# Kernel tuning notes

Measured on AMD Instinct MI355X. Metric: run time of the kernel, lower is better.

## Reference

```python
import jax, jax.numpy as jnp
import numpy as np
from jax import lax


def _conv(x, w, b):
    # 3x3 conv, stride 1, padding 1 == SAME; NCHW / OIHW layout like torch
    y = lax.conv_general_dilated(x, w, window_strides=(1, 1), padding='SAME',
                                 dimension_numbers=('NCHW', 'OIHW', 'NCHW'))
    return y + b[None, :, None, None]


def _maxpool2(x):
    return lax.reduce_window(x, -jnp.inf, lax.max, (1, 1, 2, 2), (1, 1, 2, 2), 'VALID')


def _upsample2(x):
    # nearest-neighbor upsample, scale factor 2
    return jnp.repeat(jnp.repeat(x, 2, axis=2), 2, axis=3)


def setup_inputs() -> dict:
    key = jax.random.key(0)
    ks = jax.random.split(key, 10)
    B, H, W = 128, 128, 128
    n_codes, d = 512, 32
    s = 0.1
    return {
        'x': jax.random.normal(ks[0], (B, 1, H, W), jnp.float32),
        'w1': jax.random.normal(ks[1], (16, 1, 3, 3), jnp.float32) * s,
        'b1': jnp.zeros((16,), jnp.float32),
        'w2': jax.random.normal(ks[2], (32, 16, 3, 3), jnp.float32) * s,
        'b2': jnp.zeros((32,), jnp.float32),
        'codebook': jax.random.normal(ks[3], (n_codes, d), jnp.float32),
        'w3': jax.random.normal(ks[4], (16, 32, 3, 3), jnp.float32) * s,
        'b3': jnp.zeros((16,), jnp.float32),
        'w4': jax.random.normal(ks[5], (1, 16, 3, 3), jnp.float32) * s,
        'b4': jnp.zeros((1,), jnp.float32),
    }


def reference(x, w1, b1, w2, b2, codebook, w3, b3, w4, b4):
    # encoder
    h = jax.nn.gelu(_maxpool2(_conv(x, w1, b1)), approximate=False)
    h = _maxpool2(_conv(h, w2, b2))  # [B, 32, H/4, W/4]
    B, C, Hq, Wq = h.shape

    # VectorQuantize: euclidean nearest-code lookup on flattened fmap
    z = h.transpose(0, 2, 3, 1).reshape(B, Hq * Wq, C)  # [B, N, d]
    d2 = ((z * z).sum(-1, keepdims=True)
          - 2.0 * jnp.einsum('bnc,kc->bnk', z, codebook)
          + (codebook * codebook).sum(-1))  # [B, N, K]
    idx = jnp.argmin(d2, axis=-1)  # [B, N]
    quant = codebook[idx]  # [B, N, d]
    commit_loss = jnp.mean((lax.stop_gradient(quant) - z) ** 2)
    indices = idx.reshape(B, Hq, Wq)

    # decoder: NOTE the source discards the quantized output (x_flat) and
    # keeps feeding the pre-quantization fmap h forward; we match that.
    g = jax.nn.gelu(_conv(_upsample2(h), w3, b3), approximate=False)
    out = jnp.clip(_conv(_upsample2(g), w4, b4), -1.0, 1.0)
    return out, indices, commit_loss
```

## Files before the change

### kernel.cpp

```cpp
#include <hip/hip_runtime.h>
#include <math.h>

__device__ __forceinline__ float gelu_f(float x) {
    return 0.5f * x * (1.0f + erff(x * 0.7071067811865476f));
}

__global__ __launch_bounds__(256) void k_prep(const float* __restrict__ cb,
                                              float* __restrict__ ccp) {
    const int k = blockIdx.x * 256 + threadIdx.x;
    if (k < 512) {
        const float* row = cb + k * 32;
        float s = 0.f;
#pragma unroll
        for (int c = 0; c < 32; ++c) s += row[c] * row[c];
        ccp[k] = s;
    }
}

__global__ __launch_bounds__(256) void k_conv1(const float* __restrict__ x,
                                               const float* __restrict__ w1,
                                               const float* __restrict__ b1,
                                               float* __restrict__ h1) {
    __shared__ float xs[34 * 38];
    const int blk = blockIdx.x;
    const int b = blk >> 4;
    const int tile = blk & 15;
    const int ti = (tile >> 2) << 4, tj = (tile & 3) << 4;
    const int t = threadIdx.x;
    const float* xb = x + b * 16384;
    for (int i = t; i < 34 * 34; i += 256) {
        const int r = i / 34, c = i % 34;
        const int gr = 2 * ti - 1 + r, gc = 2 * tj - 1 + c;
        const float v = ((unsigned)gr < 128u && (unsigned)gc < 128u) ? xb[gr * 128 + gc] : 0.f;
        xs[r * 38 + (c & 1) * 19 + (c >> 1)] = v;
    }
    __syncthreads();
    const int jj = t & 15, ii = t >> 4;
    float pat[4][4];
#pragma unroll
    for (int r = 0; r < 4; r++) {
        const int row = (2 * ii + r) * 38;
        pat[r][0] = xs[row + jj];
        pat[r][1] = xs[row + 19 + jj];
        pat[r][2] = xs[row + jj + 1];
        pat[r][3] = xs[row + 20 + jj];
    }
    const int obase = b * 65536 + (ti + ii) * 64 + (tj + jj);
#pragma unroll 2
    for (int co = 0; co < 16; co++) {
        const float* wr = w1 + co * 9;
        float w[9];
#pragma unroll
        for (int k = 0; k < 9; k++) w[k] = wr[k];
        float s00 = 0.f, s01 = 0.f, s10 = 0.f, s11 = 0.f;
#pragma unroll
        for (int ty = 0; ty < 3; ty++)
#pragma unroll
            for (int tx = 0; tx < 3; tx++) {
                const float wv = w[ty * 3 + tx];
                s00 += wv * pat[ty][tx];
                s01 += wv * pat[ty][tx + 1];
                s10 += wv * pat[ty + 1][tx];
                s11 += wv * pat[ty + 1][tx + 1];
            }
        const float m = fmaxf(fmaxf(s00, s01), fmaxf(s10, s11)) + b1[co];
        h1[obase + co * 4096] = gelu_f(m);
    }
}

__global__ __launch_bounds__(256) void k_conv2(const float* __restrict__ h1,
                                               const float* __restrict__ w2,
                                               const float* __restrict__ b2,
                                               float* __restrict__ h) {
    __shared__ float hs[16 * 360];
    const int blk = blockIdx.x;
    const int b = blk >> 4;
    const int tile = blk & 15;
    const int ti = (tile >> 2) << 3, tj = (tile & 3) << 3;
    const int t = threadIdx.x;
    const float* h1b = h1 + b * 65536;
    for (int i = t; i < 16 * 324; i += 256) {
        const int ci = i / 324, rc = i % 324, r = rc / 18, c = rc % 18;
        const int gr = 2 * ti - 1 + r, gc = 2 * tj - 1 + c;
        const float v = ((unsigned)gr < 64u && (unsigned)gc < 64u) ? h1b[ci * 4096 + gr * 64 + gc] : 0.f;
        hs[ci * 360 + r * 20 + (c & 1) * 10 + (c >> 1)] = v;
    }
    __syncthreads();
    const int co0 = __builtin_amdgcn_readfirstlane((t >> 6) << 3);
    const int lane = t & 63;
    const int irow = lane >> 3, j = lane & 7;
    float acc[8][4];
#pragma unroll
    for (int q = 0; q < 8; q++) { acc[q][0] = 0.f; acc[q][1] = 0.f; acc[q][2] = 0.f; acc[q][3] = 0.f; }
    const float* wbase = w2 + co0 * 144;
#pragma unroll 4
    for (int ci = 0; ci < 16; ci++) {
        float pat[4][4];
#pragma unroll
        for (int r = 0; r < 4; r++) {
            const int row = ci * 360 + (2 * irow + r) * 20;
            pat[r][0] = hs[row + j];
            pat[r][1] = hs[row + 10 + j];
            pat[r][2] = hs[row + j + 1];
            pat[r][3] = hs[row + 11 + j];
        }
#pragma unroll
        for (int q = 0; q < 8; q++) {
            const float* wr = wbase + q * 144 + ci * 9;
            float w[9];
#pragma unroll
            for (int k = 0; k < 9; k++) w[k] = wr[k];
#pragma unroll
            for (int ty = 0; ty < 3; ty++)
#pragma unroll
                for (int tx = 0; tx < 3; tx++) {
                    const float wv = w[ty * 3 + tx];
                    acc[q][0] += wv * pat[ty][tx];
                    acc[q][1] += wv * pat[ty][tx + 1];
                    acc[q][2] += wv * pat[ty + 1][tx];
                    acc[q][3] += wv * pat[ty + 1][tx + 1];
                }
        }
    }
    float* hb = h + (b * 32 + co0) * 1024 + (ti + irow) * 32 + tj + j;
#pragma unroll
    for (int q = 0; q < 8; q++) {
        hb[q * 1024] = fmaxf(fmaxf(acc[q][0], acc[q][1]), fmaxf(acc[q][2], acc[q][3])) + b2[co0 + q];
    }
}

__global__ __launch_bounds__(256) void k_vq_part(const float* __restrict__ h,
                                                 const float* __restrict__ cb,
                                                 const float* __restrict__ ccp,
                                                 float2* __restrict__ part) {
    const int blk = blockIdx.x;
    const int nchunk = blk >> 2, ks = blk & 3;
    const int t = threadIdx.x;
    const int n = nchunk * 256 + t;
    const int b = n >> 10, pos = n & 1023;
    const float* hb = h + b * 32768 + pos;
    float z[32];
    float zz = 0.f;
#pragma unroll
    for (int c = 0; c < 32; ++c) {
        z[c] = hb[c * 1024];
        zz += z[c] * z[c];
    }
    const int kbase = ks << 7;
    const float* cbb = cb + (kbase << 5);
    const float* ccb = ccp + kbase;
    float bd = 3.4e38f;
    int bk = 0;
#pragma unroll 1
    for (int kk = 0; kk < 128; kk += 2) {
        const float* r0 = cbb + (kk << 5);
        const float* r1 = r0 + 32;
        float d0a = 0.f, d0b = 0.f, d1a = 0.f, d1b = 0.f;
#pragma unroll
        for (int c = 0; c < 32; c += 2) {
            d0a += z[c] * r0[c];
            d0b += z[c + 1] * r0[c + 1];
            d1a += z[c] * r1[c];
            d1b += z[c + 1] * r1[c + 1];
        }
        const float dot0 = d0a + d0b;
        const float dot1 = d1a + d1b;
        const float e0 = (zz - 2.f * dot0) + ccb[kk];
        const float e1 = (zz - 2.f * dot1) + ccb[kk + 1];
        if (e0 < bd) { bd = e0; bk = kbase + kk; }
        if (e1 < bd) { bd = e1; bk = kbase + kk + 1; }
    }
    part[ks * 131072 + n] = make_float2(bd, (float)bk);
}

__global__ __launch_bounds__(256) void k_vq_comb(const float2* __restrict__ part,
                                                 float* __restrict__ idx_out,
                                                 float* __restrict__ partials) {
    const int t = threadIdx.x;
    const int n = blockIdx.x * 256 + t;
    float2 p0 = part[n];
    float2 p1 = part[131072 + n];
    float2 p2 = part[262144 + n];
    float2 p3 = part[393216 + n];
    float bd = p0.x;
    float bk = p0.y;
    if (p1.x < bd) { bd = p1.x; bk = p1.y; }
    if (p2.x < bd) { bd = p2.x; bk = p2.y; }
    if (p3.x < bd) { bd = p3.x; bk = p3.y; }
    idx_out[n] = bk;
    __shared__ float red[256];
    red[t] = bd;
    __syncthreads();
    for (int off = 128; off > 0; off >>= 1) {
        if (t < off) red[t] += red[t + off];
        __syncthreads();
    }
    if (t == 0) partials[blockIdx.x] = red[0];
}

__global__ __launch_bounds__(256) void k_conv3(const float* __restrict__ h,
                                               const float* __restrict__ w3,
                                               const float* __restrict__ b3,
                                               float* __restrict__ g) {
    __shared__ float hS[16 * 350];
    const int blk = blockIdx.x;
    const int b = blk >> 2, strip = blk & 3;
    const int i0 = strip * 8;
    const int t = threadIdx.x;
    const int co0 = __builtin_amdgcn_readfirstlane((t >> 6) << 2);
    const int lane = t & 63;
    const int rp = lane >> 3, cg = lane & 7;
    float acc[4][2][8];
#pragma unroll
    for (int cq = 0; cq < 4; cq++)
#pragma unroll
        for (int rr = 0; rr < 2; rr++)
#pragma unroll
            for (int u = 0; u < 8; u++) acc[cq][rr][u] = 0.f;
    const float* hb = h + b * 32768;
#pragma unroll 1
    for (int chunk = 0; chunk < 2; chunk++) {
        __syncthreads();
        for (int i = t; i < 16 * 340; i += 256) {
            const int cil = i / 340, rc = i % 340, r = rc / 34, c = rc % 34;
            const int gr = i0 - 1 + r, gc = c - 1;
            const float v = ((unsigned)gr < 32u && (unsigned)gc < 32u)
                ? hb[(chunk * 16 + cil) * 1024 + gr * 32 + gc] : 0.f;
            hS[cil * 350 + r * 35 + c] = v;
        }
        __syncthreads();
#pragma unroll 2
        for (int cil = 0; cil < 16; cil++) {
            const int ci = chunk * 16 + cil;
            float colr[3][6];
#pragma unroll
            for (int rr = 0; rr < 3; rr++) {
                const int rowb = cil * 350 + (rp + rr) * 35 + 4 * cg;
#pragma unroll
                for (int u = 0; u < 6; u++) colr[rr][u] = hS[rowb + u];
            }
#pragma unroll
            for (int cq = 0; cq < 4; cq++) {
                const float* wr = w3 + ((co0 + cq) * 32 + ci) * 9;
                float w[9];
#pragma unroll
                for (int k = 0; k < 9; k++) w[k] = wr[k];
                const float T00 = w[0], T01 = w[1], T02 = w[2];
                const float T10 = w[3] + w[6], T11 = w[4] + w[7], T12 = w[5] + w[8];
                const float T20 = w[0] + w[3], T21 = w[1] + w[4], T22 = w[2] + w[5];
                const float T30 = w[6], T31 = w[7], T32 = w[8];
                const float E01 = T01 + T02, O00 = T00 + T01;
                const float E11 = T11 + T12, O10 = T10 + T11;
                const float E21 = T21 + T22, O20 = T20 + T21;
                const float E31 = T31 + T32, O30 = T30 + T31;
#pragma unroll
                for (int mm = 0; mm < 4; mm++) {
                    acc[cq][0][2 * mm]     += T00 * colr[0][mm] + E01 * colr[0][mm + 1] + T10 * colr[1][mm] + E11 * colr[1][mm + 1];
                    acc[cq][0][2 * mm + 1] += O00 * colr[0][mm + 1] + T02 * colr[0][mm + 2] + O10 * colr[1][mm + 1] + T12 * colr[1][mm + 2];
                    acc[cq][1][2 * mm]     += T20 * colr[1][mm] + E21 * colr[1][mm + 1] + T30 * colr[2][mm] + E31 * colr[2][mm + 1];
                    acc[cq][1][2 * mm + 1] += O20 * colr[1][mm + 1] + T22 * colr[1][mm + 2] + O30 * colr[2][mm + 1] + T32 * colr[2][mm + 2];
                }
            }
        }
    }
    const int p_e = strip * 16 + 2 * rp;
#pragma unroll
    for (int cq = 0; cq < 4; cq++) {
        const float bias = b3[co0 + cq];
        float* gb = g + (b * 16 + co0 + cq) * 4096 + p_e * 64 + 8 * cg;
#pragma unroll
        for (int rr = 0; rr < 2; rr++) {
            float4 v0, v1;
            v0.x = gelu_f(acc[cq][rr][0] + bias);
            v0.y = gelu_f(acc[cq][rr][1] + bias);
            v0.z = gelu_f(acc[cq][rr][2] + bias);
            v0.w = gelu_f(acc[cq][rr][3] + bias);
            v1.x = gelu_f(acc[cq][rr][4] + bias);
            v1.y = gelu_f(acc[cq][rr][5] + bias);
            v1.z = gelu_f(acc[cq][rr][6] + bias);
            v1.w = gelu_f(acc[cq][rr][7] + bias);
            *(float4*)(gb + rr * 64) = v0;
            *(float4*)(gb + rr * 64 + 4) = v1;
        }
    }
}

__global__ __launch_bounds__(256) void k_conv4(const float* __restrict__ g,
                                               const float* __restrict__ w4,
                                               const float* __restrict__ b4,
                                               float* __restrict__ out) {
    __shared__ float gS[8 * 690];
    const int blk = blockIdx.x;
    const int b = blk >> 3, strip = blk & 7;
    const int i0 = strip * 8;
    const int t = threadIdx.x;
    const int rp = t >> 5, cg = t & 31;
    float acc[2][4];
#pragma unroll
    for (int rr = 0; rr < 2; rr++)
#pragma unroll
        for (int u = 0; u < 4; u++) acc[rr][u] = 0.f;
    const float* gbs = g + b * 65536;
#pragma unroll 1
    for (int chunk = 0; chunk < 2; chunk++) {
        __syncthreads();
        for (int i = t; i < 8 * 660; i += 256) {
            const int cil = i / 660, rc = i % 660, r = rc / 66, c = rc % 66;
            const int gr = i0 - 1 + r, gc = c - 1;
            const float v = ((unsigned)gr < 64u && (unsigned)gc < 64u)
                ? gbs[(chunk * 8 + cil) * 4096 + gr * 64 + gc] : 0.f;
            gS[cil * 690 + r * 69 + c] = v;
        }
        __syncthreads();
#pragma unroll 2
        for (int cil = 0; cil < 8; cil++) {
            const int ci = chunk * 8 + cil;
            float colv[3][4];
#pragma unroll
            for (int rr = 0; rr < 3; rr++) {
                const int rowb = cil * 690 + (rp + rr) * 69 + 2 * cg;
#pragma unroll
                for (int u = 0; u < 4; u++) colv[rr][u] = gS[rowb + u];
            }
            const float* wr = w4 + ci * 9;
            float w[9];
#pragma unroll
            for (int k = 0; k < 9; k++) w[k] = wr[k];
            const float T00 = w[0], T01 = w[1], T02 = w[2];
            const float T10 = w[3] + w[6], T11 = w[4] + w[7], T12 = w[5] + w[8];
            const float T20 = w[0] + w[3], T21 = w[1] + w[4], T22 = w[2] + w[5];
            const float T30 = w[6], T31 = w[7], T32 = w[8];
            const float E01 = T01 + T02, O00 = T00 + T01;
            const float E11 = T11 + T12, O10 = T10 + T11;
            const float E21 = T21 + T22, O20 = T20 + T21;
            const float E31 = T31 + T32, O30 = T30 + T31;
#pragma unroll
            for (int mm = 0; mm < 2; mm++) {
                acc[0][2 * mm]     += T00 * colv[0][mm] + E01 * colv[0][mm + 1] + T10 * colv[1][mm] + E11 * colv[1][mm + 1];
                acc[0][2 * mm + 1] += O00 * colv[0][mm + 1] + T02 * colv[0][mm + 2] + O10 * colv[1][mm + 1] + T12 * colv[1][mm + 2];
                acc[1][2 * mm]     += T20 * colv[1][mm] + E21 * colv[1][mm + 1] + T30 * colv[2][mm] + E31 * colv[2][mm + 1];
                acc[1][2 * mm + 1] += O20 * colv[1][mm + 1] + T22 * colv[1][mm + 2] + O30 * colv[2][mm + 1] + T32 * colv[2][mm + 2];
            }
        }
    }
    const float bias = b4[0];
    const int p_e = strip * 16 + 2 * rp;
    float* ob = out + b * 16384 + p_e * 128 + 4 * cg;
#pragma unroll
    for (int rr = 0; rr < 2; rr++) {
        float4 v;
        v.x = fminf(fmaxf(acc[rr][0] + bias, -1.f), 1.f);
        v.y = fminf(fmaxf(acc[rr][1] + bias, -1.f), 1.f);
        v.z = fminf(fmaxf(acc[rr][2] + bias, -1.f), 1.f);
        v.w = fminf(fmaxf(acc[rr][3] + bias, -1.f), 1.f);
        *(float4*)(ob + rr * 128) = v;
    }
}

__global__ __launch_bounds__(256) void k_reduce(const float* __restrict__ partials,
                                                float* __restrict__ loss) {
    __shared__ float red[256];
    const int t = threadIdx.x;
    float s = 0.f;
    for (int i = t; i < 512; i += 256) s += partials[i];
    red[t] = s;
    __syncthreads();
    for (int off = 128; off > 0; off >>= 1) {
        if (t < off) red[t] += red[t + off];
        __syncthreads();
    }
    if (t == 0) loss[0] = red[0] * (1.0f / 4194304.0f);
}

extern "C" void kernel_launch(void* const* d_in, const int* in_sizes, int n_in,
                              void* d_out, int out_size, void* d_ws, size_t ws_size,
                              hipStream_t stream) {
    const float* x  = (const float*)d_in[0];
    const float* w1 = (const float*)d_in[1];
    const float* b1 = (const float*)d_in[2];
    const float* w2 = (const float*)d_in[3];
    const float* b2 = (const float*)d_in[4];
    const float* cb = (const float*)d_in[5];
    const float* w3 = (const float*)d_in[6];
    const float* b3 = (const float*)d_in[7];
    const float* w4 = (const float*)d_in[8];
    const float* b4 = (const float*)d_in[9];

    float* ws = (float*)d_ws;
    float* h1 = ws;
    float* h  = ws + 8388608;
    float* g  = h1;
    float2* part = (float2*)ws;
    float* ccp = ws + 12582912;
    float* pa  = ws + 12583424;
    float* outp = (float*)d_out;

    k_prep<<<2, 256, 0, stream>>>(cb, ccp);
    k_conv1<<<2048, 256, 0, stream>>>(x, w1, b1, h1);
    k_conv2<<<2048, 256, 0, stream>>>(h1, w2, b2, h);
    k_vq_part<<<2048, 256, 0, stream>>>(h, cb, ccp, part);
    k_vq_comb<<<512, 256, 0, stream>>>(part, outp + 2097152, pa);
    k_conv3<<<512, 256, 0, stream>>>(h, w3, b3, g);
    k_conv4<<<1024, 256, 0, stream>>>(g, w4, b4, outp);
    k_reduce<<<1, 256, 0, stream>>>(pa, outp + 2228224);
}
```

Before: 243.0 us.

## Precompute folded upsample-conv weights and use packed float2 FMAs in conv2/VQ

Moves the folding of the 3x3 weights into upsample-aware 4x4 combinations for conv3 and conv4 out of the inner loops and into the prep kernel, which writes them to workspace. conv3 and conv4 then load 16 precomputed values per channel instead of 9 raw weights plus adds. conv2 and the VQ distance loop switch to 2-wide float vectors so the compiler can emit packed FP32 FMAs. This adds workspace traffic for the transformed weights and relies on the compiler actually emitting packed math.

Result: no change. 239.0 us (-1.7%).

```diff
diff --git a/kernel.cpp b/kernel.cpp
--- a/kernel.cpp
+++ b/kernel.cpp
@@ -1,19 +1,49 @@
 #include <hip/hip_runtime.h>
 #include <math.h>
 
+typedef float f32x2 __attribute__((ext_vector_type(2)));
+
 __device__ __forceinline__ float gelu_f(float x) {
     return 0.5f * x * (1.0f + erff(x * 0.7071067811865476f));
 }
 
 __global__ __launch_bounds__(256) void k_prep(const float* __restrict__ cb,
-                                              float* __restrict__ ccp) {
-    const int k = blockIdx.x * 256 + threadIdx.x;
-    if (k < 512) {
-        const float* row = cb + k * 32;
+                                              const float* __restrict__ w3,
+                                              const float* __restrict__ w4,
+                                              float* __restrict__ ccp,
+                                              float* __restrict__ w3t,
+                                              float* __restrict__ w4t) {
+    const int id = blockIdx.x * 256 + threadIdx.x;
+    {
+        const float* row = cb + id * 32;
         float s = 0.f;
 #pragma unroll
         for (int c = 0; c < 32; ++c) s += row[c] * row[c];
-        ccp[k] = s;
+        ccp[id] = s;
+    }
+    {
+        const float* w = w3 + id * 9;
+        const float T00 = w[0], T01 = w[1], T02 = w[2];
+        const float T10 = w[3] + w[6], T11 = w[4] + w[7], T12 = w[5] + w[8];
+        const float T20 = w[0] + w[3], T21 = w[1] + w[4], T22 = w[2] + w[5];
+        const float T30 = w[6], T31 = w[7], T32 = w[8];
+        float* o = w3t + id * 16;
+        o[0] = T00; o[1] = T00 + T01; o[2] = T01 + T02; o[3] = T02;
+        o[4] = T10; o[5] = T10 + T11; o[6] = T11 + T12; o[7] = T12;
+        o[8] = T20; o[9] = T20 + T21; o[10] = T21 + T22; o[11] = T22;
+        o[12] = T30; o[13] = T30 + T31; o[14] = T31 + T32; o[15] = T32;
+    }
+    if (id < 16) {
+        const float* w = w4 + id * 9;
+        const float T00 = w[0], T01 = w[1], T02 = w[2];
+        const float T10 = w[3] + w[6], T11 = w[4] + w[7], T12 = w[5] + w[8];
+        const float T20 = w[0] + w[3], T21 = w[1] + w[4], T22 = w[2] + w[5];
+        const float T30 = w[6], T31 = w[7], T32 = w[8];
+        float* o = w4t + id * 16;
+        o[0] = T00; o[1] = T00 + T01; o[2] = T01 + T02; o[3] = T02;
+        o[4] = T10; o[5] = T10 + T11; o[6] = T11 + T12; o[7] = T12;
+        o[8] = T20; o[9] = T20 + T21; o[10] = T21 + T22; o[11] = T22;
+        o[12] = T30; o[13] = T30 + T31; o[14] = T31 + T32; o[15] = T32;
     }
 }
 
@@ -89,20 +119,23 @@
     const int co0 = __builtin_amdgcn_readfirstlane((t >> 6) << 3);
     const int lane = t & 63;
     const int irow = lane >> 3, j = lane & 7;
-    float acc[8][4];
-#pragma unroll
-    for (int q = 0; q < 8; q++) { acc[q][0] = 0.f; acc[q][1] = 0.f; acc[q][2] = 0.f; acc[q][3] = 0.f; }
+    f32x2 A[8], B[8];
+#pragma unroll
+    for (int q = 0; q < 8; q++) { A[q] = (f32x2){0.f, 0.f}; B[q] = (f32x2){0.f, 0.f}; }
     const float* wbase = w2 + co0 * 144;
 #pragma unroll 4
     for (int ci = 0; ci < 16; ci++) {
-        float pat[4][4];
+        f32x2 P[4][3];
 #pragma unroll
         for (int r = 0; r < 4; r++) {
             const int row = ci * 360 + (2 * irow + r) * 20;
-            pat[r][0] = hs[row + j];
-            pat[r][1] = hs[row + 10 + j];
-            pat[r][2] = hs[row + j + 1];
-            pat[r][3] = hs[row + 11 + j];
+            const float e0 = hs[row + j];
+            const float o0 = hs[row + 10 + j];
+            const float e1 = hs[row + j + 1];
+            const float o1 = hs[row + 11 + j];
+            P[r][0] = (f32x2){e0, o0};
+            P[r][1] = (f32x2){o0, e1};
+            P[r][2] = (f32x2){e1, o1};
         }
 #pragma unroll
         for (int q = 0; q < 8; q++) {
@@ -115,17 +148,15 @@
 #pragma unroll
                 for (int tx = 0; tx < 3; tx++) {
                     const float wv = w[ty * 3 + tx];
-                    acc[q][0] += wv * pat[ty][tx];
-                    acc[q][1] += wv * pat[ty][tx + 1];
-                    acc[q][2] += wv * pat[ty + 1][tx];
-                    acc[q][3] += wv * pat[ty + 1][tx + 1];
+                    A[q] += P[ty][tx] * wv;
+                    B[q] += P[ty + 1][tx] * wv;
                 }
         }
     }
     float* hb = h + (b * 32 + co0) * 1024 + (ti + irow) * 32 + tj + j;
 #pragma unroll
     for (int q = 0; q < 8; q++) {
-        hb[q * 1024] = fmaxf(fmaxf(acc[q][0], acc[q][1]), fmaxf(acc[q][2], acc[q][3])) + b2[co0 + q];
+        hb[q * 1024] = fmaxf(fmaxf(A[q].x, A[q].y), fmaxf(B[q].x, B[q].y)) + b2[co0 + q];
     }
 }
 
@@ -146,6 +177,9 @@
         z[c] = hb[c * 1024];
         zz += z[c] * z[c];
     }
+    f32x2 z2[16];
+#pragma unroll
+    for (int i = 0; i < 16; ++i) z2[i] = (f32x2){z[2 * i], z[2 * i + 1]};
     const int kbase = ks << 7;
     const float* cbb = cb + (kbase << 5);
     const float* ccb = ccp + kbase;
@@ -153,18 +187,17 @@
     int bk = 0;
 #pragma unroll 1
     for (int kk = 0; kk < 128; kk += 2) {
-        const float* r0 = cbb + (kk << 5);
-        const float* r1 = r0 + 32;
-        float d0a = 0.f, d0b = 0.f, d1a = 0.f, d1b = 0.f;
-#pragma unroll
-        for (int c = 0; c < 32; c += 2) {
-            d0a += z[c] * r0[c];
-            d0b += z[c + 1] * r0[c + 1];
-            d1a += z[c] * r1[c];
-            d1b += z[c + 1] * r1[c + 1];
-        }
-        const float dot0 = d0a + d0b;
-        const float dot1 = d1a + d1b;
+        const f32x2* r0 = (const f32x2*)(cbb + (kk << 5));
+        const f32x2* r1 = (const f32x2*)(cbb + (kk << 5) + 32);
+        f32x2 D0 = (f32x2){0.f, 0.f};
+        f32x2 D1 = (f32x2){0.f, 0.f};
+#pragma unroll
+        for (int i = 0; i < 16; ++i) {
+            D0 += z2[i] * r0[i];
+            D1 += z2[i] * r1[i];
+        }
+        const float dot0 = D0.x + D0.y;
+        const float dot1 = D1.x + D1.y;
         const float e0 = (zz - 2.f * dot0) + ccb[kk];
         const float e1 = (zz - 2.f * dot1) + ccb[kk + 1];
         if (e0 < bd) { bd = e0; bk = kbase + kk; }
@@ -199,7 +232,7 @@
 }
 
 __global__ __launch_bounds__(256) void k_conv3(const float* __restrict__ h,
-                                               const float* __restrict__ w3,
+                                               const float* __restrict__ w3t,
                                                const float* __restrict__ b3,
                                                float* __restrict__ g) {
     __shared__ float hS[16 * 350];
@@ -241,18 +274,11 @@
             }
 #pragma unroll
             for (int cq = 0; cq < 4; cq++) {
-                const float* wr = w3 + ((co0 + cq) * 32 + ci) * 9;
-                float w[9];
-#pragma unroll
-                for (int k = 0; k < 9; k++) w[k] = wr[k];
-                const float T00 = w[0], T01 = w[1], T02 = w[2];
-                const float T10 = w[3] + w[6], T11 = w[4] + w[7], T12 = w[5] + w[8];
-                const float T20 = w[0] + w[3], T21 = w[1] + w[4], T22 = w[2] + w[5];
-                const float T30 = w[6], T31 = w[7], T32 = w[8];
-                const float E01 = T01 + T02, O00 = T00 + T01;
-                const float E11 = T11 + T12, O10 = T10 + T11;
-                const float E21 = T21 + T22, O20 = T20 + T21;
-                const float E31 = T31 + T32, O30 = T30 + T31;
+                const float* wt = w3t + ((co0 + cq) * 32 + ci) * 16;
+                const float T00 = wt[0], O00 = wt[1], E01 = wt[2], T02 = wt[3];
+                const float T10 = wt[4], O10 = wt[5], E11 = wt[6], T12 = wt[7];
+                const float T20 = wt[8], O20 = wt[9], E21 = wt[10], T22 = wt[11];
+                const float T30 = wt[12], O30 = wt[13], E31 = wt[14], T32 = wt[15];
 #pragma unroll
                 for (int mm = 0; mm < 4; mm++) {
                     acc[cq][0][2 * mm]     += T00 * colr[0][mm] + E01 * colr[0][mm + 1] + T10 * colr[1][mm] + E11 * colr[1][mm + 1];
@@ -286,7 +312,7 @@
 }
 
 __global__ __launch_bounds__(256) void k_conv4(const float* __restrict__ g,
-                                               const float* __restrict__ w4,
+                                               const float* __restrict__ w4t,
                                                const float* __restrict__ b4,
                                                float* __restrict__ out) {
     __shared__ float gS[8 * 690];
@@ -322,18 +348,11 @@
 #pragma unroll
                 for (int u = 0; u < 4; u++) colv[rr][u] = gS[rowb + u];
             }
-            const float* wr = w4 + ci * 9;
-            float w[9];
-#pragma unroll
-            for (int k = 0; k < 9; k++) w[k] = wr[k];
-            const float T00 = w[0], T01 = w[1], T02 = w[2];
-            const float T10 = w[3] + w[6], T11 = w[4] + w[7], T12 = w[5] + w[8];
-            const float T20 = w[0] + w[3], T21 = w[1] + w[4], T22 = w[2] + w[5];
-            const float T30 = w[6], T31 = w[7], T32 = w[8];
-            const float E01 = T01 + T02, O00 = T00 + T01;
-            const float E11 = T11 + T12, O10 = T10 + T11;
-            const float E21 = T21 + T22, O20 = T20 + T21;
-            const float E31 = T31 + T32, O30 = T30 + T31;
+            const float* wt = w4t + ci * 16;
+            const float T00 = wt[0], O00 = wt[1], E01 = wt[2], T02 = wt[3];
+            const float T10 = wt[4], O10 = wt[5], E11 = wt[6], T12 = wt[7];
+            const float T20 = wt[8], O20 = wt[9], E21 = wt[10], T22 = wt[11];
+            const float T30 = wt[12], O30 = wt[13], E31 = wt[14], T32 = wt[15];
 #pragma unroll
             for (int mm = 0; mm < 2; mm++) {
                 acc[0][2 * mm]     += T00 * colv[0][mm] + E01 * colv[0][mm + 1] + T10 * colv[1][mm] + E11 * colv[1][mm + 1];
@@ -393,14 +412,16 @@
     float2* part = (float2*)ws;
     float* ccp = ws + 12582912;
     float* pa  = ws + 12583424;
+    float* w3t = ws + 12583936;
+    float* w4t = ws + 12592128;
     float* outp = (float*)d_out;
 
-    k_prep<<<2, 256, 0, stream>>>(cb, ccp);
+    k_prep<<<2, 256, 0, stream>>>(cb, w3, w4, ccp, w3t, w4t);
     k_conv1<<<2048, 256, 0, stream>>>(x, w1, b1, h1);
     k_conv2<<<2048, 256, 0, stream>>>(h1, w2, b2, h);
     k_vq_part<<<2048, 256, 0, stream>>>(h, cb, ccp, part);
     k_vq_comb<<<512, 256, 0, stream>>>(part, outp + 2097152, pa);
-    k_conv3<<<512, 256, 0, stream>>>(h, w3, b3, g);
-    k_conv4<<<1024, 256, 0, stream>>>(g, w4, b4, outp);
+    k_conv3<<<512, 256, 0, stream>>>(h, w3t, b3, g);
+    k_conv4<<<1024, 256, 0, stream>>>(g, w4t, b4, outp);
     k_reduce<<<1, 256, 0, stream>>>(pa, outp + 2228224);
 }
```
